# Kernel optimization log

Measured on AMD Instinct MI355X. Metric: run time of the kernel, lower is better.

## Reference

```python
import jax, jax.numpy as jnp
import numpy as np

B, S, D, H, HD = 2, 4096, 768, 12, 64
W = 256           # one-sided window (attention_window=512)
C = S // W        # number of query chunks
NEG = -1e9


def _heads(x):
    # [B,S,D] -> [B,H,S,HD]
    return x.reshape(B, S, H, HD).transpose(0, 2, 1, 3)


def setup_inputs() -> dict:
    key = jax.random.key(0)
    ks = jax.random.split(key, 9)
    sc = 0.02
    w = lambda i: jax.random.normal(ks[i], (D, D), jnp.float32) * sc
    return {
        "hidden_states": jax.random.normal(ks[0], (B, S, D), jnp.float32),
        "Wq": w(1), "Wk": w(2), "Wv": w(3),
        "Wqg": w(4), "Wkg": w(5), "Wvg": w(6),
        "Wo": w(7),
        "attention_mask": jnp.ones((B, S), jnp.int32),
    }


def reference(hidden_states, Wq, Wk, Wv, Wqg, Wkg, Wvg, Wo, attention_mask):
    x = hidden_states
    scale = 1.0 / float(np.sqrt(HD))
    q = _heads(x @ Wq) * scale           # [B,H,S,HD]
    k = _heads(x @ Wk)
    v = _heads(x @ Wv)

    # ---- banded sliding-window attention (chunked, no [S,S] matrix) ----
    idx = jnp.arange(C)[:, None] * W + jnp.arange(3 * W)[None, :]   # [C,3W] into padded seq
    key_pos = idx - W                                               # absolute key position
    kp = jnp.pad(k, ((0, 0), (0, 0), (W, W), (0, 0)))
    vp = jnp.pad(v, ((0, 0), (0, 0), (W, W), (0, 0)))
    kc = kp[:, :, idx]                   # [B,H,C,3W,HD]
    vc = vp[:, :, idx]
    qc = q.reshape(B, H, C, W, HD)
    band = jnp.einsum('bhcqd,bhckd->bhcqk', qc, kc)  # [B,H,C,W,3W]

    qi = jnp.arange(W)[:, None]
    kj = jnp.arange(3 * W)[None, :]
    diag_ok = (kj >= qi) & (kj <= qi + 2 * W)              # |i-j| <= W
    valid = (key_pos >= 0) & (key_pos < S) & (key_pos != 0)  # in-range, dedupe global key 0
    mask = diag_ok[None, :, :] & valid[:, None, :]          # [C,W,3W]
    band = jnp.where(mask[None, None], band, NEG)

    # padding mask on keys
    m = jnp.where(attention_mask > 0, 0.0, NEG).astype(jnp.float32)  # [B,S]
    mp = jnp.pad(m, ((0, 0), (W, W)), constant_values=NEG)
    band = band + mp[:, idx][:, None, :, None, :]
    band = band.reshape(B, H, S, 3 * W)

    # every local query also attends to the global (CLS, pos 0) key
    gsc = jnp.einsum('bhsd,bhgd->bhsg', q, k[:, :, 0:1])   # [B,H,S,1]
    gsc = gsc + m[:, 0][:, None, None, None]

    scores = jnp.concatenate([gsc, band], axis=-1)          # [B,H,S,1+3W]
    probs = jax.nn.softmax(scores, axis=-1)
    pg = probs[..., :1]                                     # global-key prob
    pb = probs[..., 1:].reshape(B, H, C, W, 3 * W)
    out = jnp.einsum('bhcqk,bhckd->bhcqd', pb, vc).reshape(B, H, S, HD)
    out = out + pg * v[:, :, 0:1]

    # ---- global query (CLS) full attention with dedicated projections ----
    qg = _heads(x @ Wqg)[:, :, 0:1] * scale                 # [B,H,1,HD]
    kg = _heads(x @ Wkg)
    vg = _heads(x @ Wvg)
    gs = jnp.einsum('bhgd,bhsd->bhgs', qg, kg) + m[:, None, None, :]
    og = jnp.einsum('bhgs,bhsd->bhgd', jax.nn.softmax(gs, axis=-1), vg)
    out = out.at[:, :, 0:1].set(og)

    out = out.transpose(0, 2, 1, 3).reshape(B, S, D) @ Wo
    return out
```

## Files before the change

kernel.cpp:

```cpp
#include <hip/hip_runtime.h>

#define S_LEN 4096
#define NH 12
#define HDIM 64
#define DMODEL 768
#define NEGF -1.0e9f
#define TOK0_SPLITS 16

typedef __attribute__((ext_vector_type(8))) short bf16x8;
typedef __attribute__((ext_vector_type(4))) float f32x4;

__device__ __forceinline__ short f2b(float f) {
  union { float f; unsigned u; } v; v.f = f;
  unsigned r = v.u + 0x7fffu + ((v.u >> 16) & 1u);
  return (short)(r >> 16);
}
__device__ __forceinline__ float b2f(short s) {
  union { unsigned u; float f; } v; v.u = ((unsigned)(unsigned short)s) << 16;
  return v.f;
}

__global__ __launch_bounds__(256) void k_pre(const float* __restrict__ x,
                                             const float* __restrict__ Wq,
                                             const float* __restrict__ Wk,
                                             const float* __restrict__ Wv,
                                             const float* __restrict__ Wkg,
                                             const float* __restrict__ Wvg,
                                             const float* __restrict__ Wo,
                                             const float* __restrict__ Wqg,
                                             const int* __restrict__ amask,
                                             short* __restrict__ xb,
                                             short* __restrict__ W5t,
                                             short* __restrict__ Wot,
                                             float* __restrict__ qg,
                                             float* __restrict__ mvb) {
  __shared__ float smem[1056];
  int bid = blockIdx.x, tid = threadIdx.x;
  if (bid < 6144) {
    int i = bid * 256 + tid;
    float4 v = ((const float4*)x)[i];
    ((short4*)xb)[i] = make_short4(f2b(v.x), f2b(v.y), f2b(v.z), f2b(v.w));
  } else if (bid < 9600) {
    int zb = bid - 6144;
    int z = zb / 576, rem = zb - z * 576;
    int by = rem / 24, bx = rem - by * 24;
    const float* src; float scale = 1.f; short* dst;
    switch (z) {
      case 0: src = Wq;  scale = 0.125f * 1.44269504f; dst = W5t; break;
      case 1: src = Wk;  dst = W5t + 589824; break;
      case 2: src = Wv;  dst = W5t + 2 * 589824; break;
      case 3: src = Wkg; dst = W5t + 3 * 589824; break;
      case 4: src = Wvg; dst = W5t + 4 * 589824; break;
      default: src = Wo; dst = Wot; break;
    }
    int tx = tid & 31, ty = tid >> 5;
    int kb = by * 32, nb = bx * 32;
    for (int i = 0; i < 4; i++) smem[(ty + 8 * i) * 33 + tx] = src[(kb + ty + 8 * i) * 768 + nb + tx];
    __syncthreads();
    for (int i = 0; i < 4; i++)
      dst[(nb + ty + 8 * i) * 768 + kb + tx] = f2b(smem[tx * 33 + ty + 8 * i] * scale);
  } else if (bid < 9632) {
    int zb = bid - 9600;
    int b = zb >> 4, s = (zb & 15) * 256 + tid;
    mvb[b * S_LEN + s] = (s != 0 && amask[b * S_LEN + s] > 0) ? 0.f : NEGF;
  } else {
    int zb = bid - 9632;
    int h = zb % 12, b = zb / 12;
    int out = tid & 63, slice = tid >> 6;
    float* xr = smem;
    float* ps = smem + 768;
    for (int i = tid; i < 768; i += 256) xr[i] = x[(long)b * S_LEN * 768 + i];
    __syncthreads();
    float a = 0.f;
    int n = h * 64 + out;
#pragma unroll 8
    for (int k = slice * 192; k < slice * 192 + 192; k++) a += xr[k] * Wqg[k * 768 + n];
    ps[slice * 64 + out] = a;
    __syncthreads();
    if (tid < 64)
      qg[b * 768 + h * 64 + tid] = (ps[tid] + ps[64 + tid] + ps[128 + tid] + ps[192 + tid]) * 0.125f;
  }
}

__global__ __launch_bounds__(256) void k_gemm(const short* __restrict__ A,
                                              const short* __restrict__ Bt, int K, int mode,
                                              short* __restrict__ qkv, float* __restrict__ outf) {
  __shared__ short Al[2][128 * 32];
  __shared__ short Bl[2][128 * 32];
  int bid = blockIdx.x;
  int xcd = bid & 7, ii = bid >> 3;
  int bm = xcd * 8 + (ii & 7), bn = ii >> 3;
  int tid = threadIdx.x;
  int bm0 = bm * 128, bn0 = bn * 128;
  int w = tid >> 6, lane = tid & 63, g = lane >> 4, r16 = lane & 15;
  int wr = (w >> 1) * 64, wc = (w & 1) * 64;
  f32x4 zero4 = {0.f, 0.f, 0.f, 0.f};
  f32x4 acc[4][4];
  for (int m = 0; m < 4; m++) for (int n = 0; n < 4; n++) acc[m][n] = zero4;
  int srow = w * 32 + (lane >> 2);
  int scol = (lane & 3) * 8;
#define G_STAGE(BUF, KT)                                                              \
  do {                                                                                \
    for (int i = 0; i < 2; i++) {                                                     \
      const short* ga = &A[(long)(bm0 + srow + i * 16) * K + (KT) + scol];            \
      const short* gb = &Bt[(long)(bn0 + srow + i * 16) * K + (KT) + scol];           \
      __builtin_amdgcn_global_load_lds(                                               \
          (const __attribute__((address_space(1))) void*)ga,                          \
          (__attribute__((address_space(3))) void*)&Al[BUF][(w * 32 + i * 16) * 32],  \
          16, 0, 0);                                                                  \
      __builtin_amdgcn_global_load_lds(                                               \
          (const __attribute__((address_space(1))) void*)gb,                          \
          (__attribute__((address_space(3))) void*)&Bl[BUF][(w * 32 + i * 16) * 32],  \
          16, 0, 0);                                                                  \
    }                                                                                 \
  } while (0)
  int nt = K >> 5;
  G_STAGE(0, 0);
  __syncthreads();
  int cur = 0;
  for (int t = 0; t < nt; t++) {
    if (t + 1 < nt) G_STAGE(cur ^ 1, (t + 1) * 32);
    bf16x8 af[4], bfv[4];
    for (int m = 0; m < 4; m++) af[m] = *(const bf16x8*)&Al[cur][(wr + m * 16 + r16) * 32 + g * 8];
    for (int n = 0; n < 4; n++) bfv[n] = *(const bf16x8*)&Bl[cur][(wc + n * 16 + r16) * 32 + g * 8];
    for (int m = 0; m < 4; m++)
      for (int n = 0; n < 4; n++)
        acc[m][n] = __builtin_amdgcn_mfma_f32_16x16x32_bf16(af[m], bfv[n], acc[m][n], 0, 0, 0);
    __syncthreads();
    cur ^= 1;
  }
#undef G_STAGE
  for (int m = 0; m < 4; m++)
    for (int n = 0; n < 4; n++)
      for (int reg = 0; reg < 4; reg++) {
        int row = bm0 + wr + m * 16 + g * 4 + reg;
        int col = bn0 + wc + n * 16 + r16;
        float val = acc[m][n][reg];
        if (mode == 0) {
          int proj = col / 768;
          int rem = col - proj * 768;
          int hh = rem >> 6, d = rem & 63;
          int bb = row >> 12, s = row & 4095;
          qkv[(long)proj * 6291456 + ((((long)bb * NH + hh) * S_LEN + s) << 6) + d] = f2b(val);
        } else {
          outf[(long)row * 768 + col] = val;
        }
      }
}

__global__ __launch_bounds__(256) void k_vt(const short* __restrict__ V, short* __restrict__ Vt) {
  __shared__ short buf[64][72];
  int st = blockIdx.x, bh = blockIdx.y;
  int tid = threadIdx.x;
  long base = (long)bh * S_LEN * HDIM;
  int s0 = st * 64;
  int r = tid >> 2, c = (tid & 3) * 16;
  *(int4*)&buf[r][c]     = *(const int4*)&V[base + (long)(s0 + r) * HDIM + c];
  *(int4*)&buf[r][c + 8] = *(const int4*)&V[base + (long)(s0 + r) * HDIM + c + 8];
  __syncthreads();
  int d = tid >> 2, sc = (tid & 3) * 16;
  short tmp[16];
#pragma unroll
  for (int j = 0; j < 16; j++) tmp[j] = buf[sc + j][d];
  long ob = base + (long)d * S_LEN + s0 + sc;
  *(int4*)&Vt[ob]     = *(const int4*)&tmp[0];
  *(int4*)&Vt[ob + 8] = *(const int4*)&tmp[8];
}

#define KVPAD 36
#define PSTRIDE 68

__device__ __forceinline__ void band_chunk(
    int ks0, int qrow0, int g, int r16,
    const bf16x8 (&qf)[2][2], const bf16x8 (&kf)[4][2], const bf16x8 (&vf)[4][2],
    const float (&mv)[4],
    float (&mstate)[2][4], float (&lstate)[2][4], f32x4 (&acc)[2][4],
    short* Plds) {
  int dlo = ks0 - qrow0;
  bool fullok = (dlo >= -224) && (dlo <= 192);
  for (int m = 0; m < 2; m++) {
    f32x4 s[4];
    f32x4 zero4 = {0.f, 0.f, 0.f, 0.f};
    for (int n = 0; n < 4; n++) {
      f32x4 z = __builtin_amdgcn_mfma_f32_16x16x32_bf16(qf[m][0], kf[n][0], zero4, 0, 0, 0);
      s[n] = __builtin_amdgcn_mfma_f32_16x16x32_bf16(qf[m][1], kf[n][1], z, 0, 0, 0);
    }
    float p[4][4], rmax[4];
    for (int reg = 0; reg < 4; reg++) rmax[reg] = NEGF;
    if (fullok) {
      for (int n = 0; n < 4; n++)
        for (int reg = 0; reg < 4; reg++) {
          float val = s[n][reg] + mv[n];
          p[n][reg] = val;
          rmax[reg] = fmaxf(rmax[reg], val);
        }
    } else {
      int qbase = qrow0 + m * 16 + g * 4;
      for (int n = 0; n < 4; n++) {
        int kpos = ks0 + n * 16 + r16;
        for (int reg = 0; reg < 4; reg++) {
          int qpos = qbase + reg;
          bool ok = (kpos >= qpos - 256) && (kpos <= qpos + 256);
          float val = ok ? (s[n][reg] + mv[n]) : NEGF;
          p[n][reg] = val;
          rmax[reg] = fmaxf(rmax[reg], val);
        }
      }
    }
    for (int reg = 0; reg < 4; reg++) {
      float r = rmax[reg];
      r = fmaxf(r, __shfl_xor(r, 1));
      r = fmaxf(r, __shfl_xor(r, 2));
      r = fmaxf(r, __shfl_xor(r, 4));
      r = fmaxf(r, __shfl_xor(r, 8));
      rmax[reg] = r;
    }
    bool over = false;
    for (int reg = 0; reg < 4; reg++) over = over || (rmax[reg] > mstate[m][reg] + 8.f);
    if (__any((int)over)) {
      float scal[4];
      for (int reg = 0; reg < 4; reg++) {
        float mn = fmaxf(mstate[m][reg], rmax[reg]);
        scal[reg] = __builtin_amdgcn_exp2f(mstate[m][reg] - mn);
        mstate[m][reg] = mn;
      }
      float rs[4] = {0.f, 0.f, 0.f, 0.f};
      for (int n = 0; n < 4; n++)
        for (int reg = 0; reg < 4; reg++) {
          float e = __builtin_amdgcn_exp2f(p[n][reg] - mstate[m][reg]);
          p[n][reg] = e;
          rs[reg] += e;
        }
      for (int reg = 0; reg < 4; reg++) {
        float r = rs[reg];
        r += __shfl_xor(r, 1);
        r += __shfl_xor(r, 2);
        r += __shfl_xor(r, 4);
        r += __shfl_xor(r, 8);
        lstate[m][reg] = lstate[m][reg] * scal[reg] + r;
      }
      for (int n = 0; n < 4; n++)
        for (int reg = 0; reg < 4; reg++) acc[m][n][reg] *= scal[reg];
    } else {
      float rs[4] = {0.f, 0.f, 0.f, 0.f};
      for (int n = 0; n < 4; n++)
        for (int reg = 0; reg < 4; reg++) {
          float e = __builtin_amdgcn_exp2f(p[n][reg] - mstate[m][reg]);
          p[n][reg] = e;
          rs[reg] += e;
        }
      for (int reg = 0; reg < 4; reg++) {
        float r = rs[reg];
        r += __shfl_xor(r, 1);
        r += __shfl_xor(r, 2);
        r += __shfl_xor(r, 4);
        r += __shfl_xor(r, 8);
        lstate[m][reg] += r;
      }
    }
    for (int n = 0; n < 4; n++)
      for (int reg = 0; reg < 4; reg++)
        Plds[(g * 4 + reg) * PSTRIDE + n * 16 + r16] = f2b(p[n][reg]);
    bf16x8 pa[2];
    for (int ks = 0; ks < 2; ks++)
      pa[ks] = *(const bf16x8*)&Plds[r16 * PSTRIDE + ks * 32 + g * 8];
    for (int n = 0; n < 4; n++)
      for (int ks = 0; ks < 2; ks++)
        acc[m][n] = __builtin_amdgcn_mfma_f32_16x16x32_bf16(pa[ks], vf[n][ks], acc[m][n], 0, 0, 0);
  }
}

__global__ __launch_bounds__(256, 2) void k_attn(const short* __restrict__ Qb,
                                                 const short* __restrict__ Kb,
                                                 const short* __restrict__ Vb,
                                                 const short* __restrict__ Vtb,
                                                 const short* __restrict__ Kg,
                                                 const short* __restrict__ Vg,
                                                 const float* __restrict__ qg,
                                                 const int* __restrict__ amask,
                                                 const float* __restrict__ mvb,
                                                 short* __restrict__ oattn,
                                                 float* __restrict__ part) {
  __shared__ short Klds[2][2][64][KVPAD];
  __shared__ short Plds[4][16 * PSTRIDE];
  __shared__ float fsm[592];
  int bid = blockIdx.x, tid = threadIdx.x;
  if (bid < 768) {
    int qtb = bid & 31, rest = bid >> 5;
    int h = rest % NH, b = rest / NH;
    int w = tid >> 6, lane = tid & 63, g = lane >> 4, r16 = lane & 15;
    long bhof = ((long)(b * NH + h)) * S_LEN * HDIM;
    int qb0 = qtb * 128;
    int qrow0 = qb0 + w * 32;

    bf16x8 qf[2][2];
    for (int m = 0; m < 2; m++)
      for (int ks = 0; ks < 2; ks++)
        qf[m][ks] = *(const bf16x8*)&Qb[bhof + (long)(qrow0 + m * 16 + r16) * HDIM + ks * 32 + g * 8];

    float mstate[2][4], lstate[2][4];
    f32x4 acc[2][4];
    {
      bf16x8 k0f[2];
      for (int ks = 0; ks < 2; ks++) k0f[ks] = *(const bf16x8*)&Kb[bhof + ks * 32 + g * 8];
      float part0[2];
      for (int m = 0; m < 2; m++) {
        float p = 0.f;
        for (int ks = 0; ks < 2; ks++)
          for (int j = 0; j < 8; j++) p += b2f(qf[m][ks][j]) * b2f(k0f[ks][j]);
        p += __shfl_xor(p, 16);
        p += __shfl_xor(p, 32);
        part0[m] = p;
      }
      float mask0 = (amask[b * S_LEN] > 0) ? 0.f : NEGF;
      float v0v[4];
      for (int n = 0; n < 4; n++) v0v[n] = b2f(Vb[bhof + n * 16 + r16]);
      for (int m = 0; m < 2; m++)
        for (int reg = 0; reg < 4; reg++) {
          mstate[m][reg] = __shfl(part0[m], g * 4 + reg) + mask0;
          lstate[m][reg] = 1.f;
          for (int n = 0; n < 4; n++) acc[m][n][reg] = v0v[n];
        }
    }

    int c0 = (qb0 - 256) >> 6; if (c0 < 0) c0 = 0;
    int c1 = (qb0 + 127 + 256) >> 6; if (c1 > 63) c1 = 63;
    int wlo = (qrow0 - 256) >> 6;
    int whi = (qrow0 + 31 + 256) >> 6;

    int ss = tid >> 2, qq = tid & 3;
    int ksh = qq >> 1, qcol = (qq & 1) * 16;
    int4 rk0, rk1;
#define STAGE_LOAD(CI)                                                              \
    do {                                                                            \
      int _k = (CI) * 64;                                                           \
      const int4* gk = (const int4*)&Kb[bhof + (long)(_k + ss) * HDIM + qq * 16];   \
      rk0 = gk[0]; rk1 = gk[1];                                                     \
    } while (0)
#define STAGE_WRITE(BUF)                                                            \
    do {                                                                            \
      short* kd = &Klds[BUF][ksh][ss][qcol];                                        \
      *(int4*)kd = rk0; *(int4*)(kd + 8) = rk1;                                     \
    } while (0)

    STAGE_LOAD(c0);
    STAGE_WRITE(0);
    __syncthreads();

    for (int ci = c0; ci <= c1; ci++) {
      int buf = (ci - c0) & 1;
      bool havenext = (ci + 1 <= c1);
      if (havenext) STAGE_LOAD(ci + 1);
      if (ci >= wlo && ci <= whi) {
        int ks0 = ci * 64;
        bf16x8 vf[4][2];
        for (int n = 0; n < 4; n++)
          for (int ks = 0; ks < 2; ks++)
            vf[n][ks] = *(const bf16x8*)&Vtb[bhof + (long)(n * 16 + r16) * S_LEN + ks0 + ks * 32 + g * 8];
        float mv[4];
        for (int n = 0; n < 4; n++) mv[n] = mvb[b * S_LEN + ks0 + n * 16 + r16];
        bf16x8 kf[4][2];
        for (int n = 0; n < 4; n++)
          for (int ks = 0; ks < 2; ks++)
            kf[n][ks] = *(const bf16x8*)&Klds[buf][ks][n * 16 + r16][g * 8];
        band_chunk(ks0, qrow0, g, r16, qf, kf, vf, mv, mstate, lstate, acc, &Plds[w][0]);
      }
      if (havenext) STAGE_WRITE(buf ^ 1);
      __syncthreads();
    }
#undef STAGE_LOAD
#undef STAGE_WRITE

    for (int m = 0; m < 2; m++)
      for (int n = 0; n < 4; n++)
        for (int reg = 0; reg < 4; reg++) {
          int token = qrow0 + m * 16 + g * 4 + reg;
          int col = h * 64 + n * 16 + r16;
          oattn[((long)b * S_LEN + token) * 768 + col] = f2b(acc[m][n][reg] / lstate[m][reg]);
        }
  } else {
    int tbid = bid - 768;
    int split = tbid & 15, bhid = tbid >> 4;
    int b = bhid / NH, h = bhid % NH;
    long base = (long)bhid * S_LEN * HDIM;
    int lane = tid & 63, w = tid >> 6;
    int s = split * 256 + tid;
    float* qgl  = fsm;
    float* p_sh = fsm + 64;
    float* red  = fsm + 320;
    float* psum = fsm + 324;
    if (tid < 64) qgl[tid] = qg[b * 768 + h * 64 + tid];
    __syncthreads();
    float dot = 0.f;
    {
      const int4* kr = (const int4*)&Kg[base + (long)s * HDIM];
#pragma unroll
      for (int u = 0; u < 8; u++) {
        int4 pk = kr[u];
        const short* sp = (const short*)&pk;
        for (int j = 0; j < 8; j++) dot += qgl[u * 8 + j] * b2f(sp[j]);
      }
      dot += (amask[b * S_LEN + s] > 0) ? 0.f : NEGF;
    }
    float mx = dot;
    for (int o = 32; o; o >>= 1) mx = fmaxf(mx, __shfl_xor(mx, o));
    if (lane == 0) red[w] = mx;
    __syncthreads();
    mx = fmaxf(fmaxf(red[0], red[1]), fmaxf(red[2], red[3]));
    float e = __expf(dot - mx);
    p_sh[tid] = e;
    float sum = e;
    for (int o = 32; o; o >>= 1) sum += __shfl_xor(sum, o);
    __syncthreads();
    if (lane == 0) red[w] = sum;
    __syncthreads();
    sum = red[0] + red[1] + red[2] + red[3];
    int d = tid & 63, grp = tid >> 6;
    float a = 0.f;
    long vb = base + (long)(split * 256 + grp * 64) * HDIM + d;
#pragma unroll 8
    for (int j = 0; j < 64; j++) a += p_sh[grp * 64 + j] * b2f(Vg[vb + (long)j * HDIM]);
    psum[grp * 64 + d] = a;
    __syncthreads();
    float* dst = &part[((long)bhid * TOK0_SPLITS + split) * 66];
    if (tid == 0) { dst[0] = mx; dst[1] = sum; }
    if (tid < 64)
      dst[2 + tid] = psum[tid] + psum[64 + tid] + psum[128 + tid] + psum[192 + tid];
  }
}

__global__ void k_tok0_comb(const float* __restrict__ part, short* __restrict__ oattn) {
  int bhid = blockIdx.x, d = threadIdx.x;
  int b = bhid / NH, h = bhid % NH;
  const float* p0 = &part[(long)bhid * TOK0_SPLITS * 66];
  float M = NEGF;
  for (int i = 0; i < TOK0_SPLITS; i++) M = fmaxf(M, p0[i * 66]);
  float L = 0.f, a = 0.f;
  for (int i = 0; i < TOK0_SPLITS; i++) {
    float sc = __expf(p0[i * 66] - M);
    L += sc * p0[i * 66 + 1];
    a += sc * p0[i * 66 + 2 + d];
  }
  oattn[((long)b * S_LEN) * 768 + h * 64 + d] = f2b(a / L);
}

extern "C" void kernel_launch(void* const* d_in, const int* in_sizes, int n_in,
                              void* d_out, int out_size, void* d_ws, size_t ws_size,
                              hipStream_t stream) {
  (void)in_sizes; (void)n_in; (void)out_size; (void)ws_size;
  const float* x   = (const float*)d_in[0];
  const float* Wq  = (const float*)d_in[1];
  const float* Wk  = (const float*)d_in[2];
  const float* Wv  = (const float*)d_in[3];
  const float* Wqg = (const float*)d_in[4];
  const float* Wkg = (const float*)d_in[5];
  const float* Wvg = (const float*)d_in[6];
  const float* Wo  = (const float*)d_in[7];
  const int* amask = (const int*)d_in[8];
  char* ws = (char*)d_ws;
  short* xb    = (short*)(ws);
  short* Vt    = (short*)(ws);
  short* W5t   = (short*)(ws + 12582912);
  short* Wot   = (short*)(ws + 18481152);
  short* qkv   = (short*)(ws + 19660800);
  short* oattn = (short*)(ws + 82575360);
  float* qgbuf = (float*)(ws + 95158272);
  float* partb = (float*)(ws + 95164416);
  float* mvb   = (float*)(ws + 95265792);
  float* outf  = (float*)d_out;

  k_pre<<<9656, 256, 0, stream>>>(x, Wq, Wk, Wv, Wkg, Wvg, Wo, Wqg, amask,
                                  xb, W5t, Wot, qgbuf, mvb);
  k_gemm<<<1920, 256, 0, stream>>>(xb, W5t, 768, 0, qkv, nullptr);
  const short* Qb = qkv;
  const short* Kb = qkv + 6291456;
  const short* Vb = qkv + 2 * 6291456;
  const short* Kg = qkv + 3 * 6291456;
  const short* Vg = qkv + 4 * 6291456;
  k_vt<<<dim3(64, 24), 256, 0, stream>>>(Vb, Vt);
  k_attn<<<1152, 256, 0, stream>>>(Qb, Kb, Vb, Vt, Kg, Vg, qgbuf, amask, mvb, oattn, partb);
  k_tok0_comb<<<24, 64, 0, stream>>>(partb, oattn);
  k_gemm<<<384, 256, 0, stream>>>(oattn, Wot, 768, 1, nullptr, outf);
}
```

Baseline: 208.9 us.

## Split key chunks across wave pairs and merge softmax states via LDS

Each attention block now covers 64 query rows instead of 128. Two waves share each 32-row query slice and take alternating key chunks, then merge their online-softmax states (max, sum, accumulator) through shared memory before writing the output. The shared-LDS K double buffer and its per-chunk block barriers are removed, and K fragments are read straight from global memory. This doubles the number of attention blocks to raise parallelism and shorten each wave's serial chain. The cost is redundant global K loads, a larger merge buffer in LDS, and an extra merge step. The merge uses exp2 on state values, which may or may not match the base used inside band_chunk.

```diff
diff --git a/kernel.cpp b/kernel.cpp
--- a/kernel.cpp
+++ b/kernel.cpp
@@ -167,7 +167,6 @@
   *(int4*)&Vt[ob + 8] = *(const int4*)&tmp[8];
 }
 
-#define KVPAD 36
 #define PSTRIDE 68
 
 __device__ __forceinline__ void band_chunk(
@@ -281,17 +280,18 @@
                                                  const float* __restrict__ mvb,
                                                  short* __restrict__ oattn,
                                                  float* __restrict__ part) {
-  __shared__ short Klds[2][2][64][KVPAD];
   __shared__ short Plds[4][16 * PSTRIDE];
+  __shared__ float mrg[2][48][65];
   __shared__ float fsm[592];
   int bid = blockIdx.x, tid = threadIdx.x;
-  if (bid < 768) {
-    int qtb = bid & 31, rest = bid >> 5;
+  if (bid < 1536) {
+    int qt = bid & 63, rest = bid >> 6;
     int h = rest % NH, b = rest / NH;
     int w = tid >> 6, lane = tid & 63, g = lane >> 4, r16 = lane & 15;
+    int pair = w >> 1;
+    int par = w & 1;
     long bhof = ((long)(b * NH + h)) * S_LEN * HDIM;
-    int qb0 = qtb * 128;
-    int qrow0 = qb0 + w * 32;
+    int qrow0 = qt * 64 + pair * 32;
 
     bf16x8 qf[2][2];
     for (int m = 0; m < 2; m++)
@@ -300,7 +300,7 @@
 
     float mstate[2][4], lstate[2][4];
     f32x4 acc[2][4];
-    {
+    if (par == 0) {
       bf16x8 k0f[2];
       for (int ks = 0; ks < 2; ks++) k0f[ks] = *(const bf16x8*)&Kb[bhof + ks * 32 + g * 8];
       float part0[2];
@@ -321,65 +321,60 @@
           lstate[m][reg] = 1.f;
           for (int n = 0; n < 4; n++) acc[m][n][reg] = v0v[n];
         }
-    }
-
-    int c0 = (qb0 - 256) >> 6; if (c0 < 0) c0 = 0;
-    int c1 = (qb0 + 127 + 256) >> 6; if (c1 > 63) c1 = 63;
-    int wlo = (qrow0 - 256) >> 6;
-    int whi = (qrow0 + 31 + 256) >> 6;
-
-    int ss = tid >> 2, qq = tid & 3;
-    int ksh = qq >> 1, qcol = (qq & 1) * 16;
-    int4 rk0, rk1;
-#define STAGE_LOAD(CI)                                                              \
-    do {                                                                            \
-      int _k = (CI) * 64;                                                           \
-      const int4* gk = (const int4*)&Kb[bhof + (long)(_k + ss) * HDIM + qq * 16];   \
-      rk0 = gk[0]; rk1 = gk[1];                                                     \
-    } while (0)
-#define STAGE_WRITE(BUF)                                                            \
-    do {                                                                            \
-      short* kd = &Klds[BUF][ksh][ss][qcol];                                        \
-      *(int4*)kd = rk0; *(int4*)(kd + 8) = rk1;                                     \
-    } while (0)
-
-    STAGE_LOAD(c0);
-    STAGE_WRITE(0);
-    __syncthreads();
-
-    for (int ci = c0; ci <= c1; ci++) {
-      int buf = (ci - c0) & 1;
-      bool havenext = (ci + 1 <= c1);
-      if (havenext) STAGE_LOAD(ci + 1);
-      if (ci >= wlo && ci <= whi) {
-        int ks0 = ci * 64;
-        bf16x8 vf[4][2];
-        for (int n = 0; n < 4; n++)
-          for (int ks = 0; ks < 2; ks++)
-            vf[n][ks] = *(const bf16x8*)&Vtb[bhof + (long)(n * 16 + r16) * S_LEN + ks0 + ks * 32 + g * 8];
-        float mv[4];
-        for (int n = 0; n < 4; n++) mv[n] = mvb[b * S_LEN + ks0 + n * 16 + r16];
-        bf16x8 kf[4][2];
-        for (int n = 0; n < 4; n++)
-          for (int ks = 0; ks < 2; ks++)
-            kf[n][ks] = *(const bf16x8*)&Klds[buf][ks][n * 16 + r16][g * 8];
-        band_chunk(ks0, qrow0, g, r16, qf, kf, vf, mv, mstate, lstate, acc, &Plds[w][0]);
-      }
-      if (havenext) STAGE_WRITE(buf ^ 1);
-      __syncthreads();
-    }
-#undef STAGE_LOAD
-#undef STAGE_WRITE
-
-    for (int m = 0; m < 2; m++)
-      for (int n = 0; n < 4; n++)
-        for (int reg = 0; reg < 4; reg++) {
+    } else {
+      for (int m = 0; m < 2; m++)
+        for (int reg = 0; reg < 4; reg++) {
+          mstate[m][reg] = NEGF;
+          lstate[m][reg] = 0.f;
+          for (int n = 0; n < 4; n++) acc[m][n][reg] = 0.f;
+        }
+    }
+
+    int wlo = (qrow0 - 256) >> 6; if (wlo < 0) wlo = 0;
+    int whi = (qrow0 + 31 + 256) >> 6; if (whi > 63) whi = 63;
+
+    for (int ci = wlo + par; ci <= whi; ci += 2) {
+      int ks0 = ci * 64;
+      bf16x8 vf[4][2], kf[4][2];
+      for (int n = 0; n < 4; n++)
+        for (int ks = 0; ks < 2; ks++) {
+          vf[n][ks] = *(const bf16x8*)&Vtb[bhof + (long)(n * 16 + r16) * S_LEN + ks0 + ks * 32 + g * 8];
+          kf[n][ks] = *(const bf16x8*)&Kb[bhof + (long)(ks0 + n * 16 + r16) * HDIM + ks * 32 + g * 8];
+        }
+      float mv[4];
+      for (int n = 0; n < 4; n++) mv[n] = mvb[b * S_LEN + ks0 + n * 16 + r16];
+      band_chunk(ks0, qrow0, g, r16, qf, kf, vf, mv, mstate, lstate, acc, &Plds[w][0]);
+    }
+
+    if (par == 1) {
+      for (int m = 0; m < 2; m++)
+        for (int reg = 0; reg < 4; reg++) {
+          mrg[pair][m * 4 + reg][lane] = mstate[m][reg];
+          mrg[pair][8 + m * 4 + reg][lane] = lstate[m][reg];
+          for (int n = 0; n < 4; n++)
+            mrg[pair][16 + m * 16 + n * 4 + reg][lane] = acc[m][n][reg];
+        }
+    }
+    __syncthreads();
+    if (par == 0) {
+      for (int m = 0; m < 2; m++)
+        for (int reg = 0; reg < 4; reg++) {
+          float mB = mrg[pair][m * 4 + reg][lane];
+          float lB = mrg[pair][8 + m * 4 + reg][lane];
+          float M = fmaxf(mstate[m][reg], mB);
+          float sA = __builtin_amdgcn_exp2f(mstate[m][reg] - M);
+          float sB = __builtin_amdgcn_exp2f(mB - M);
+          float l = lstate[m][reg] * sA + lB * sB;
           int token = qrow0 + m * 16 + g * 4 + reg;
-          int col = h * 64 + n * 16 + r16;
-          oattn[((long)b * S_LEN + token) * 768 + col] = f2b(acc[m][n][reg] / lstate[m][reg]);
-        }
+          for (int n = 0; n < 4; n++) {
+            float a = acc[m][n][reg] * sA + mrg[pair][16 + m * 16 + n * 4 + reg][lane] * sB;
+            int col = h * 64 + n * 16 + r16;
+            oattn[((long)b * S_LEN + token) * 768 + col] = f2b(a / l);
+          }
+        }
+    }
   } else {
-    int tbid = bid - 768;
+    int tbid = bid - 1536;
     int split = tbid & 15, bhid = tbid >> 4;
     int b = bhid / NH, h = bhid % NH;
     long base = (long)bhid * S_LEN * HDIM;
@@ -478,7 +473,7 @@
   const short* Kg = qkv + 3 * 6291456;
   const short* Vg = qkv + 4 * 6291456;
   k_vt<<<dim3(64, 24), 256, 0, stream>>>(Vb, Vt);
-  k_attn<<<1152, 256, 0, stream>>>(Qb, Kb, Vb, Vt, Kg, Vg, qgbuf, amask, mvb, oattn, partb);
+  k_attn<<<1920, 256, 0, stream>>>(Qb, Kb, Vb, Vt, Kg, Vg, qgbuf, amask, mvb, oattn, partb);
   k_tok0_comb<<<24, 64, 0, stream>>>(partb, oattn);
   k_gemm<<<384, 256, 0, stream>>>(oattn, Wot, 768, 1, nullptr, outf);
 }
```

Result: faster. 200.8 us (-3.9%).
